# Kernel optimization log

Measured on AMD Instinct MI355X. Metric: run time of the kernel, lower is better.

## Reference

```python
import jax, jax.numpy as jnp
import numpy as np

DIM = 512
HEADS = 8
DIM_HEAD = 64
INNER = HEADS * DIM_HEAD  # 512
NUM_PATCHES = 64
NUM_FRAMES = 32
EPS = 1e-5


def setup_inputs() -> dict:
    key = jax.random.key(0)
    k1, k2, k3, k4 = jax.random.split(key, 4)
    B, T = 4, NUM_PATCHES * NUM_FRAMES  # 4, 2048
    x = jax.random.normal(k1, (B, T, DIM), dtype=jnp.float32)
    w_qkv = jax.random.normal(k2, (DIM, 3 * INNER), dtype=jnp.float32) * (DIM ** -0.5)
    w_out = jax.random.normal(k3, (INNER, DIM), dtype=jnp.float32) * (INNER ** -0.5)
    b_out = jax.random.normal(k4, (DIM,), dtype=jnp.float32) * 0.01
    ln_g = jnp.ones((DIM,), dtype=jnp.float32)
    ln_b = jnp.zeros((DIM,), dtype=jnp.float32)
    return {"x": x, "ln_g": ln_g, "ln_b": ln_b, "w_qkv": w_qkv, "w_out": w_out, "b_out": b_out}


def _frame_causal_mask(T):
    # token i belongs to frame i // NUM_PATCHES; query frame attends to frames <= its own
    frame = jnp.arange(T) // NUM_PATCHES
    return frame[:, None] >= frame[None, :]  # [T, T] bool


def reference(x, ln_g, ln_b, w_qkv, w_out, b_out):
    B, T, C = x.shape
    scale = DIM_HEAD ** -0.5
    # LayerNorm
    mu = jnp.mean(x, axis=-1, keepdims=True)
    var = jnp.mean(jnp.square(x - mu), axis=-1, keepdims=True)
    xn = (x - mu) * jax.lax.rsqrt(var + EPS) * ln_g + ln_b
    # QKV projection (no bias)
    qkv = xn @ w_qkv  # [B, T, 3*INNER]
    q, k, v = jnp.split(qkv, 3, axis=-1)
    reshape = lambda t: t.reshape(B, T, HEADS, DIM_HEAD).transpose(0, 2, 1, 3)  # b h n d
    q, k, v = reshape(q), reshape(k), reshape(v)
    dots = jnp.einsum('bhqd,bhkd->bhqk', q, k) * scale
    mask = _frame_causal_mask(T)
    dots = jnp.where(mask[None, None], dots, -jnp.inf)
    attn = jax.nn.softmax(dots, axis=-1)
    out = jnp.einsum('bhqk,bhkd->bhqd', attn, v)
    out = out.transpose(0, 2, 1, 3).reshape(B, T, INNER)
    return out @ w_out + b_out
```

## Files before the change

### kernel.cpp

```cpp
#include <hip/hip_runtime.h>

typedef unsigned short u16;
typedef float f32x4 __attribute__((ext_vector_type(4)));
typedef short bf16x8 __attribute__((ext_vector_type(8)));

#define MFMA16(a, b, c) __builtin_amdgcn_mfma_f32_16x16x32_bf16((a), (b), (c), 0, 0, 0)
#define SWZ8(row, off) ((off) ^ (((row) & 7) << 3))

#define CFENCE() asm volatile("" ::: "memory")
#define BARRIER() do { CFENCE(); __builtin_amdgcn_s_barrier(); CFENCE(); } while (0)
#define VMW(n) asm volatile("s_waitcnt vmcnt(" #n ")" ::: "memory")

static __device__ __forceinline__ u16 f2bf(float f) {
  union { float f; unsigned u; } c; c.f = f;
  unsigned r = c.u + 0x7fffu + ((c.u >> 16) & 1u);
  return (u16)(r >> 16);
}

static __device__ __forceinline__ void llds16(u16* l, const u16* g) {
  __builtin_amdgcn_global_load_lds((const __attribute__((address_space(1))) void*)g,
                                   (__attribute__((address_space(3))) void*)l, 16, 0, 0);
}

__global__ __launch_bounds__(256) void prep_weights(
    const float* __restrict__ w_qkv, const float* __restrict__ w_out,
    u16* __restrict__ wqkvT, u16* __restrict__ woutT) {
  int idx = blockIdx.x * 256 + threadIdx.x;
  if (idx < 1536 * 512) {
    int n = idx >> 9, k = idx & 511;
    wqkvT[idx] = f2bf(w_qkv[k * 1536 + n]);
  } else {
    int j = idx - 1536 * 512;
    int n = j >> 9, k = j & 511;
    woutT[j] = f2bf(w_out[k * 512 + n]);
  }
}

__global__ __launch_bounds__(256) void ln_kernel(
    const float* __restrict__ x, const float* __restrict__ g,
    const float* __restrict__ be, u16* __restrict__ xn) {
  int row = blockIdx.x;
  int t = threadIdx.x;
  const float* xr = x + (size_t)row * 512;
  float2 v = *(const float2*)(xr + t * 2);
  float s = v.x + v.y, ss = v.x * v.x + v.y * v.y;
#pragma unroll
  for (int msk = 32; msk >= 1; msk >>= 1) {
    s += __shfl_xor(s, msk, 64);
    ss += __shfl_xor(ss, msk, 64);
  }
  __shared__ float red[8];
  int wv = t >> 6;
  if ((t & 63) == 0) { red[wv] = s; red[4 + wv] = ss; }
  __syncthreads();
  s = red[0] + red[1] + red[2] + red[3];
  ss = red[4] + red[5] + red[6] + red[7];
  float mu = s * (1.f / 512.f);
  float var = ss * (1.f / 512.f) - mu * mu;
  float rs = rsqrtf(var + 1e-5f);
  float a0 = (v.x - mu) * rs * g[2 * t] + be[2 * t];
  float a1 = (v.y - mu) * rs * g[2 * t + 1] + be[2 * t + 1];
  u16* o = xn + (size_t)row * 512 + t * 2;
  o[0] = f2bf(a0);
  o[1] = f2bf(a1);
}

__global__ __launch_bounds__(256) void gemm_qkv(
    const u16* __restrict__ A, const u16* __restrict__ BT,
    u16* __restrict__ qb, u16* __restrict__ kb, u16* __restrict__ vtb) {
  __shared__ u16 lsA[128 * 64], lsB[128 * 64];
  int m0 = blockIdx.x * 128, n0 = blockIdx.y * 128;
  int tid = threadIdx.x;
  int lane = tid & 63, wave = tid >> 6;
  int wm = (wave >> 1) * 64, wn = (wave & 1) * 64;
  int lr = lane & 15, lq = lane >> 4;
  f32x4 acc[4][4] = {};
  for (int kt = 0; kt < 8; ++kt) {
#pragma unroll
    for (int c = 0; c < 4; ++c) {
      int ci = c * 256 + tid;
      int row = ci >> 3, colb = ci & 7;
      int goff = kt * 64 + ((colb * 8) ^ ((row & 7) * 8));
      llds16(&lsA[ci * 8], &A[(size_t)(m0 + row) * 512 + goff]);
      llds16(&lsB[ci * 8], &BT[(size_t)(n0 + row) * 512 + goff]);
    }
    __syncthreads();
#pragma unroll
    for (int ks = 0; ks < 2; ++ks) {
      bf16x8 af[4], bfr[4];
#pragma unroll
      for (int i = 0; i < 4; ++i) {
        int ra = wm + i * 16 + lr;
        af[i] = *(const bf16x8*)&lsA[ra * 64 + SWZ8(ra, ks * 32 + lq * 8)];
        int rb = wn + i * 16 + lr;
        bfr[i] = *(const bf16x8*)&lsB[rb * 64 + SWZ8(rb, ks * 32 + lq * 8)];
      }
#pragma unroll
      for (int i = 0; i < 4; ++i)
#pragma unroll
        for (int j = 0; j < 4; ++j)
          acc[i][j] = MFMA16(af[i], bfr[j], acc[i][j]);
    }
    __syncthreads();
  }
#pragma unroll
  for (int j = 0; j < 4; ++j) {
    int gn = n0 + wn + j * 16 + lr;
    int sec = gn >> 9;
    int h = (gn >> 6) & 7;
    int d = gn & 63;
#pragma unroll
    for (int i = 0; i < 4; ++i) {
      int gm = m0 + wm + i * 16 + lq * 4;
      int b = gm >> 11, t0 = gm & 2047;
      int bh = b * 8 + h;
      if (sec == 0) {
#pragma unroll
        for (int r = 0; r < 4; ++r)
          qb[((size_t)bh * 2048 + t0 + r) * 64 + d] = f2bf(acc[i][j][r] * 0.125f);
      } else if (sec == 1) {
#pragma unroll
        for (int r = 0; r < 4; ++r)
          kb[((size_t)bh * 2048 + t0 + r) * 64 + d] = f2bf(acc[i][j][r]);
      } else {
        ushort4 pk;
        pk.x = f2bf(acc[i][j][0]);
        pk.y = f2bf(acc[i][j][1]);
        pk.z = f2bf(acc[i][j][2]);
        pk.w = f2bf(acc[i][j][3]);
        *(ushort4*)&vtb[((size_t)bh * 64 + d) * 2048 + t0] = pk;
      }
    }
  }
}

__global__ __launch_bounds__(256) void attn_kernel(
    const u16* __restrict__ qb, const u16* __restrict__ kb,
    const u16* __restrict__ vtb, u16* __restrict__ ao) {
  int blk = blockIdx.x;
  int xcd = blk & 7;
  int seq = blk >> 3;
  int bh = xcd * 4 + (seq & 3);
  int qf = 31 - (seq >> 2);
  int tid = threadIdx.x, lane = tid & 63, wave = tid >> 6;
  int lr = lane & 15, lq = lane >> 4;
  __shared__ u16 lsK[2][64 * 64], lsV[2][64 * 64];
  __shared__ u16 lsP[4][16 * 64];
  const u16* kfb = kb + (size_t)bh * 2048 * 64;
  const u16* vfb = vtb + (size_t)bh * 64 * 2048;

  int ci0 = tid, ci1 = 256 + tid;
  int r0 = ci0 >> 3, cb0 = ci0 & 7, sw0 = (cb0 * 8) ^ ((r0 & 7) * 8);
  int r1 = ci1 >> 3, cb1 = ci1 & 7, sw1 = (cb1 * 8) ^ ((r1 & 7) * 8);

#define STAGE(buf, kf_)                                                        \
  do {                                                                         \
    const u16* kp = kfb + (size_t)(kf_) * 64 * 64;                             \
    llds16(&lsK[buf][ci0 * 8], &kp[(size_t)r0 * 64 + sw0]);                    \
    llds16(&lsK[buf][ci1 * 8], &kp[(size_t)r1 * 64 + sw1]);                    \
    llds16(&lsV[buf][ci0 * 8], &vfb[(size_t)r0 * 2048 + (kf_) * 64 + sw0]);    \
    llds16(&lsV[buf][ci1 * 8], &vfb[(size_t)r1 * 2048 + (kf_) * 64 + sw1]);    \
  } while (0)

  STAGE(0, 0);

  const u16* qbase = qb + ((size_t)bh * 2048 + qf * 64) * 64;
  int qrow = wave * 16 + lr;
  bf16x8 qa0 = *(const bf16x8*)&qbase[qrow * 64 + lq * 8];
  bf16x8 qa1 = *(const bf16x8*)&qbase[qrow * 64 + 32 + lq * 8];

  f32x4 o[4] = {};
  float m[4], l[4];
#pragma unroll
  for (int r = 0; r < 4; ++r) { m[r] = -1e30f; l[r] = 0.f; }

  for (int kf = 0; kf <= qf; ++kf) {
    int cur = kf & 1;
    if (kf < qf) {
      STAGE(cur ^ 1, kf + 1);
      VMW(4);
    } else {
      VMW(0);
    }
    BARRIER();
    f32x4 s[4];
#pragma unroll
    for (int c = 0; c < 4; ++c) {
      int rk = c * 16 + lr;
      bf16x8 b0 = *(const bf16x8*)&lsK[cur][rk * 64 + SWZ8(rk, lq * 8)];
      bf16x8 b1 = *(const bf16x8*)&lsK[cur][rk * 64 + SWZ8(rk, 32 + lq * 8)];
      f32x4 z = {};
      z = MFMA16(qa0, b0, z);
      z = MFMA16(qa1, b1, z);
      s[c] = z;
    }
    float al[4];
#pragma unroll
    for (int r = 0; r < 4; ++r) {
      float v = fmaxf(fmaxf(s[0][r], s[1][r]), fmaxf(s[2][r], s[3][r]));
      v = fmaxf(v, __shfl_xor(v, 1, 16));
      v = fmaxf(v, __shfl_xor(v, 2, 16));
      v = fmaxf(v, __shfl_xor(v, 4, 16));
      v = fmaxf(v, __shfl_xor(v, 8, 16));
      float mn = fmaxf(m[r], v);
      al[r] = __expf(m[r] - mn);
      m[r] = mn;
    }
#pragma unroll
    for (int c = 0; c < 4; ++c)
#pragma unroll
      for (int r = 0; r < 4; ++r)
        s[c][r] = __expf(s[c][r] - m[r]);
#pragma unroll
    for (int r = 0; r < 4; ++r) {
      float v = s[0][r] + s[1][r] + s[2][r] + s[3][r];
      v += __shfl_xor(v, 1, 16);
      v += __shfl_xor(v, 2, 16);
      v += __shfl_xor(v, 4, 16);
      v += __shfl_xor(v, 8, 16);
      l[r] = l[r] * al[r] + v;
    }
#pragma unroll
    for (int oc = 0; oc < 4; ++oc)
#pragma unroll
      for (int r = 0; r < 4; ++r)
        o[oc][r] *= al[r];
    u16* pw = lsP[wave];
#pragma unroll
    for (int c = 0; c < 4; ++c)
#pragma unroll
      for (int r = 0; r < 4; ++r) {
        int q = lq * 4 + r;
        pw[q * 64 + ((c * 16 + lr) ^ ((q & 7) << 3))] = f2bf(s[c][r]);
      }
    bf16x8 pa0 = *(const bf16x8*)&pw[lr * 64 + SWZ8(lr, lq * 8)];
    bf16x8 pa1 = *(const bf16x8*)&pw[lr * 64 + SWZ8(lr, 32 + lq * 8)];
#pragma unroll
    for (int oc = 0; oc < 4; ++oc) {
      int rv = oc * 16 + lr;
      bf16x8 v0 = *(const bf16x8*)&lsV[cur][rv * 64 + SWZ8(rv, lq * 8)];
      bf16x8 v1 = *(const bf16x8*)&lsV[cur][rv * 64 + SWZ8(rv, 32 + lq * 8)];
      o[oc] = MFMA16(pa0, v0, o[oc]);
      o[oc] = MFMA16(pa1, v1, o[oc]);
    }
    BARRIER();
  }
#undef STAGE
  int b = bh >> 3, h = bh & 7;
#pragma unroll
  for (int oc = 0; oc < 4; ++oc) {
#pragma unroll
    for (int r = 0; r < 4; ++r) {
      int q = qf * 64 + wave * 16 + lq * 4 + r;
      int col = h * 64 + oc * 16 + lr;
      ao[((size_t)b * 2048 + q) * 512 + col] = f2bf(o[oc][r] / l[r]);
    }
  }
}

__global__ __launch_bounds__(256) void gemm_out(
    const u16* __restrict__ A, const u16* __restrict__ BT,
    const float* __restrict__ bias, float* __restrict__ out) {
  __shared__ u16 lsA[128 * 64], lsB[128 * 64];
  int m0 = blockIdx.x * 128, n0 = blockIdx.y * 128;
  int tid = threadIdx.x;
  int lane = tid & 63, wave = tid >> 6;
  int wm = (wave >> 1) * 64, wn = (wave & 1) * 64;
  int lr = lane & 15, lq = lane >> 4;
  f32x4 acc[4][4] = {};
  for (int kt = 0; kt < 8; ++kt) {
#pragma unroll
    for (int c = 0; c < 4; ++c) {
      int ci = c * 256 + tid;
      int row = ci >> 3, colb = ci & 7;
      int goff = kt * 64 + ((colb * 8) ^ ((row & 7) * 8));
      llds16(&lsA[ci * 8], &A[(size_t)(m0 + row) * 512 + goff]);
      llds16(&lsB[ci * 8], &BT[(size_t)(n0 + row) * 512 + goff]);
    }
    __syncthreads();
#pragma unroll
    for (int ks = 0; ks < 2; ++ks) {
      bf16x8 af[4], bfr[4];
#pragma unroll
      for (int i = 0; i < 4; ++i) {
        int ra = wm + i * 16 + lr;
        af[i] = *(const bf16x8*)&lsA[ra * 64 + SWZ8(ra, ks * 32 + lq * 8)];
        int rb = wn + i * 16 + lr;
        bfr[i] = *(const bf16x8*)&lsB[rb * 64 + SWZ8(rb, ks * 32 + lq * 8)];
      }
#pragma unroll
      for (int i = 0; i < 4; ++i)
#pragma unroll
        for (int j = 0; j < 4; ++j)
          acc[i][j] = MFMA16(af[i], bfr[j], acc[i][j]);
    }
    __syncthreads();
  }
#pragma unroll
  for (int j = 0; j < 4; ++j) {
    int gn = n0 + wn + j * 16 + lr;
    float bj = bias[gn];
#pragma unroll
    for (int i = 0; i < 4; ++i) {
      int gm = m0 + wm + i * 16 + lq * 4;
#pragma unroll
      for (int r = 0; r < 4; ++r)
        out[(size_t)(gm + r) * 512 + gn] = acc[i][j][r] + bj;
    }
  }
}

extern "C" void kernel_launch(void* const* d_in, const int* in_sizes, int n_in,
                              void* d_out, int out_size, void* d_ws, size_t ws_size,
                              hipStream_t stream) {
  const float* x = (const float*)d_in[0];
  const float* ln_g = (const float*)d_in[1];
  const float* ln_b = (const float*)d_in[2];
  const float* w_qkv = (const float*)d_in[3];
  const float* w_out = (const float*)d_in[4];
  const float* b_out = (const float*)d_in[5];
  float* out = (float*)d_out;
  char* ws = (char*)d_ws;

  u16* xn    = (u16*)(ws + 0);
  u16* wqkvT = (u16*)(ws + 8388608);
  u16* woutT = (u16*)(ws + 9961472);
  u16* qb    = (u16*)(ws + 10485760);
  u16* kb    = (u16*)(ws + 18874368);
  u16* vtb   = (u16*)(ws + 27262976);
  u16* ao    = (u16*)(ws + 35651584);

  prep_weights<<<4096, 256, 0, stream>>>(w_qkv, w_out, wqkvT, woutT);
  ln_kernel<<<8192, 256, 0, stream>>>(x, ln_g, ln_b, xn);
  gemm_qkv<<<dim3(64, 12), 256, 0, stream>>>(xn, wqkvT, qb, kb, vtb);
  attn_kernel<<<1024, 256, 0, stream>>>(qb, kb, vtb, ao);
  gemm_out<<<dim3(64, 4), 256, 0, stream>>>(ao, woutT, b_out, out);
}
```

Baseline: 187.2 us.

## Compute transposed S tile so softmax row stats need fewer cross-lane shuffles

Swaps the MFMA operand order for QK^T so each lane holds scores for one query row across its four accumulator slots. Row max and sum then reduce over 16 values plus two shuffles, instead of four separate 16-lane shuffle trees. The P tile is packed into 64-bit LDS stores, and the per-row rescale and final normalisation use broadcasts via __shfl. It also raises wave priority around the MFMA blocks with s_setprio, which changes scheduling and may help or hurt overlap.

```diff
diff --git a/kernel.cpp b/kernel.cpp
--- a/kernel.cpp
+++ b/kernel.cpp
@@ -170,9 +170,7 @@
   bf16x8 qa1 = *(const bf16x8*)&qbase[qrow * 64 + 32 + lq * 8];
 
   f32x4 o[4] = {};
-  float m[4], l[4];
-#pragma unroll
-  for (int r = 0; r < 4; ++r) { m[r] = -1e30f; l[r] = 0.f; }
+  float m = -1e30f, l = 0.f;
 
   for (int kf = 0; kf <= qf; ++kf) {
     int cur = kf & 1;
@@ -184,57 +182,65 @@
     }
     BARRIER();
     f32x4 s[4];
+    __builtin_amdgcn_s_setprio(1);
 #pragma unroll
     for (int c = 0; c < 4; ++c) {
       int rk = c * 16 + lr;
-      bf16x8 b0 = *(const bf16x8*)&lsK[cur][rk * 64 + SWZ8(rk, lq * 8)];
-      bf16x8 b1 = *(const bf16x8*)&lsK[cur][rk * 64 + SWZ8(rk, 32 + lq * 8)];
+      bf16x8 k0 = *(const bf16x8*)&lsK[cur][rk * 64 + SWZ8(rk, lq * 8)];
+      bf16x8 k1 = *(const bf16x8*)&lsK[cur][rk * 64 + SWZ8(rk, 32 + lq * 8)];
       f32x4 z = {};
-      z = MFMA16(qa0, b0, z);
-      z = MFMA16(qa1, b1, z);
+      z = MFMA16(k0, qa0, z);
+      z = MFMA16(k1, qa1, z);
       s[c] = z;
     }
-    float al[4];
-#pragma unroll
-    for (int r = 0; r < 4; ++r) {
-      float v = fmaxf(fmaxf(s[0][r], s[1][r]), fmaxf(s[2][r], s[3][r]));
-      v = fmaxf(v, __shfl_xor(v, 1, 16));
-      v = fmaxf(v, __shfl_xor(v, 2, 16));
-      v = fmaxf(v, __shfl_xor(v, 4, 16));
-      v = fmaxf(v, __shfl_xor(v, 8, 16));
-      float mn = fmaxf(m[r], v);
-      al[r] = __expf(m[r] - mn);
-      m[r] = mn;
-    }
-#pragma unroll
-    for (int c = 0; c < 4; ++c)
-#pragma unroll
-      for (int r = 0; r < 4; ++r)
-        s[c][r] = __expf(s[c][r] - m[r]);
-#pragma unroll
-    for (int r = 0; r < 4; ++r) {
-      float v = s[0][r] + s[1][r] + s[2][r] + s[3][r];
-      v += __shfl_xor(v, 1, 16);
-      v += __shfl_xor(v, 2, 16);
-      v += __shfl_xor(v, 4, 16);
-      v += __shfl_xor(v, 8, 16);
-      l[r] = l[r] * al[r] + v;
-    }
-#pragma unroll
-    for (int oc = 0; oc < 4; ++oc)
-#pragma unroll
-      for (int r = 0; r < 4; ++r)
-        o[oc][r] *= al[r];
+    __builtin_amdgcn_s_setprio(0);
+    float m0 = fmaxf(fmaxf(s[0][0], s[0][1]), fmaxf(s[0][2], s[0][3]));
+    float m1 = fmaxf(fmaxf(s[1][0], s[1][1]), fmaxf(s[1][2], s[1][3]));
+    float m2 = fmaxf(fmaxf(s[2][0], s[2][1]), fmaxf(s[2][2], s[2][3]));
+    float m3 = fmaxf(fmaxf(s[3][0], s[3][1]), fmaxf(s[3][2], s[3][3]));
+    float mx = fmaxf(fmaxf(m0, m1), fmaxf(m2, m3));
+    mx = fmaxf(mx, __shfl_xor(mx, 16, 64));
+    mx = fmaxf(mx, __shfl_xor(mx, 32, 64));
+    float mn = fmaxf(m, mx);
+    float al = __expf(m - mn);
+    m = mn;
+    float sum = 0.f;
+#pragma unroll
+    for (int c = 0; c < 4; ++c) {
+#pragma unroll
+      for (int r = 0; r < 4; ++r) {
+        s[c][r] = __expf(s[c][r] - mn);
+        sum += s[c][r];
+      }
+    }
+    sum += __shfl_xor(sum, 16, 64);
+    sum += __shfl_xor(sum, 32, 64);
+    l = l * al + sum;
+    float al0 = __shfl(al, lq * 4 + 0, 64);
+    float al1 = __shfl(al, lq * 4 + 1, 64);
+    float al2 = __shfl(al, lq * 4 + 2, 64);
+    float al3 = __shfl(al, lq * 4 + 3, 64);
+#pragma unroll
+    for (int oc = 0; oc < 4; ++oc) {
+      o[oc][0] *= al0;
+      o[oc][1] *= al1;
+      o[oc][2] *= al2;
+      o[oc][3] *= al3;
+    }
     u16* pw = lsP[wave];
 #pragma unroll
-    for (int c = 0; c < 4; ++c)
-#pragma unroll
-      for (int r = 0; r < 4; ++r) {
-        int q = lq * 4 + r;
-        pw[q * 64 + ((c * 16 + lr) ^ ((q & 7) << 3))] = f2bf(s[c][r]);
-      }
+    for (int c = 0; c < 4; ++c) {
+      union { u16 h[4]; uint2 q2; } pk;
+      pk.h[0] = f2bf(s[c][0]);
+      pk.h[1] = f2bf(s[c][1]);
+      pk.h[2] = f2bf(s[c][2]);
+      pk.h[3] = f2bf(s[c][3]);
+      int kbase = c * 16 + lq * 4;
+      *(uint2*)&pw[lr * 64 + (kbase ^ ((lr & 7) * 8))] = pk.q2;
+    }
     bf16x8 pa0 = *(const bf16x8*)&pw[lr * 64 + SWZ8(lr, lq * 8)];
     bf16x8 pa1 = *(const bf16x8*)&pw[lr * 64 + SWZ8(lr, 32 + lq * 8)];
+    __builtin_amdgcn_s_setprio(1);
 #pragma unroll
     for (int oc = 0; oc < 4; ++oc) {
       int rv = oc * 16 + lr;
@@ -243,18 +249,24 @@
       o[oc] = MFMA16(pa0, v0, o[oc]);
       o[oc] = MFMA16(pa1, v1, o[oc]);
     }
+    __builtin_amdgcn_s_setprio(0);
     BARRIER();
   }
 #undef STAGE
+  float inv = 1.0f / l;
+  float i0 = __shfl(inv, lq * 4 + 0, 64);
+  float i1 = __shfl(inv, lq * 4 + 1, 64);
+  float i2 = __shfl(inv, lq * 4 + 2, 64);
+  float i3 = __shfl(inv, lq * 4 + 3, 64);
   int b = bh >> 3, h = bh & 7;
 #pragma unroll
   for (int oc = 0; oc < 4; ++oc) {
-#pragma unroll
-    for (int r = 0; r < 4; ++r) {
-      int q = qf * 64 + wave * 16 + lq * 4 + r;
-      int col = h * 64 + oc * 16 + lr;
-      ao[((size_t)b * 2048 + q) * 512 + col] = f2bf(o[oc][r] / l[r]);
-    }
+    int q = qf * 64 + wave * 16 + lq * 4;
+    int col = h * 64 + oc * 16 + lr;
+    ao[((size_t)b * 2048 + q + 0) * 512 + col] = f2bf(o[oc][0] * i0);
+    ao[((size_t)b * 2048 + q + 1) * 512 + col] = f2bf(o[oc][1] * i1);
+    ao[((size_t)b * 2048 + q + 2) * 512 + col] = f2bf(o[oc][2] * i2);
+    ao[((size_t)b * 2048 + q + 3) * 512 + col] = f2bf(o[oc][3] * i3);
   }
 }
 
```

Result: faster. 169.8 us (-9.3%).
